# Kernel tuning notes

Measured on AMD Instinct MI355X. Metric: run time of the kernel, lower is better.

## Reference

```python
import jax, jax.numpy as jnp
import numpy as np

D = 1024      # input_dim
NH = 16       # num_heads
HD = D // NH  # head_dim = 64
B, S = 2, 2048


def setup_inputs() -> dict:
    key = jax.random.key(0)
    ks = jax.random.split(key, 12)
    scale = 1.0 / np.sqrt(D)
    inp = {
        "query": jax.random.normal(ks[0], (B, S, D), jnp.float32),
        "key": jax.random.normal(ks[1], (B, S, D), jnp.float32),
        "value": jax.random.normal(ks[2], (B, S, D), jnp.float32),
        # Linear weights stored as [in, out] so y = x @ W + b
        "Wq": jax.random.normal(ks[3], (D, D), jnp.float32) * scale,
        "bq": jnp.zeros((D,), jnp.float32),
        "Wk": jax.random.normal(ks[4], (D, D), jnp.float32) * scale,
        "bk": jnp.zeros((D,), jnp.float32),
        "Wv": jax.random.normal(ks[5], (D, D), jnp.float32) * scale,
        "bv": jnp.zeros((D,), jnp.float32),
        "Wo": jax.random.normal(ks[6], (D, D), jnp.float32) * scale,
        "bo": jnp.zeros((D,), jnp.float32),
    }
    return inp


def reference(query, key, value, Wq, bq, Wk, bk, Wv, bv, Wo, bo):
    b, s, _ = query.shape
    q = query @ Wq + bq
    k = key @ Wk + bk
    v = value @ Wv + bv
    # NOTE: module reshapes to (b, s, head_dim, num_heads) -- heads LAST
    q = q.reshape(b, s, HD, NH)
    k = k.reshape(b, s, HD, NH)
    v = v.reshape(b, s, HD, NH)
    # contract over head_dim d; result [b, l, n, h]
    scores = jnp.einsum('bldh,bndh->blnh', q, k) / jnp.sqrt(jnp.float32(HD))
    # Softmax(dim=-1) in the original acts over the HEAD axis (faithful)
    probs = jax.nn.softmax(scores, axis=-1)
    out = jnp.einsum('blnh,bndh->bldh', probs, v).reshape(b, s, D)
    out = out @ Wo + bo
    return (out, probs)
```

## Files before the change

### kernel.cpp

```cpp
#include <hip/hip_runtime.h>

#define DD   1024
#define NHH  16
#define HDD  64
#define BB   2
#define SS   2048
#define MT   (BB*SS)
#define BL   16
#define BN   32
#define NSPLIT 2

typedef __attribute__((ext_vector_type(8))) __bf16 bf16x8;
typedef __attribute__((ext_vector_type(4))) float  floatx4;
typedef __attribute__((ext_vector_type(4))) short  shortx4;

static __device__ __forceinline__ short bf16_of(float f) {
    unsigned u = __builtin_bit_cast(unsigned, f);
    u = (u + 0x7fffu + ((u >> 16) & 1u)) >> 16;
    return (short)u;
}

static __device__ __forceinline__ void async_copy16(const short* g, short* l) {
    __builtin_amdgcn_global_load_lds(
        (const __attribute__((address_space(1))) unsigned int*)g,
        (__attribute__((address_space(3))) unsigned int*)l,
        16, 0, 0);
}

__global__ void cast_f32_to_bf16(const float* __restrict__ in,
                                 short* __restrict__ out, int n4) {
    int i = blockIdx.x * blockDim.x + threadIdx.x;
    if (i >= n4) return;
    floatx4 f = ((const floatx4*)in)[i];
    shortx4 o;
    o[0] = bf16_of(f[0]); o[1] = bf16_of(f[1]);
    o[2] = bf16_of(f[2]); o[3] = bf16_of(f[3]);
    ((shortx4*)out)[i] = o;
}

__global__ void transpose_cast_w(const float* __restrict__ W,
                                 short* __restrict__ Wt) {
    __shared__ float tile[32][33];
    int tx = threadIdx.x & 31, ty = threadIdx.x >> 5;
    int o0 = blockIdx.x * 32, i0 = blockIdx.y * 32;
#pragma unroll
    for (int r = 0; r < 32; r += 8)
        tile[ty + r][tx] = W[(size_t)(i0 + ty + r) * DD + o0 + tx];
    __syncthreads();
#pragma unroll
    for (int r = 0; r < 32; r += 8)
        Wt[(size_t)(o0 + ty + r) * DD + i0 + tx] = bf16_of(tile[tx][ty + r]);
}

__global__ __launch_bounds__(256) void gemm_tiled(
    const short* __restrict__ X, const short* __restrict__ Wt,
    const float* __restrict__ bias, void* __restrict__ out, int mode) {
    __shared__ short As[128 * 32];
    __shared__ short Bs[64 * 32];
    int t = threadIdx.x;
    int wave = t >> 6, lane = t & 63;
    int quad = lane >> 4, lr = lane & 15;
    int wm = wave & 1, wn = wave >> 1;
    int m0 = blockIdx.x * 128, n0 = blockIdx.y * 64;

    int arow = t >> 2, acol = (t & 3) * 8;
    floatx4 acc[4][2] = {};

    for (int k0 = 0; k0 < DD; k0 += 32) {
        async_copy16(X + (size_t)(m0 + arow) * DD + k0 + acol,       As + t * 8);
        async_copy16(X + (size_t)(m0 + 64 + arow) * DD + k0 + acol,  As + 2048 + t * 8);
        async_copy16(Wt + (size_t)(n0 + arow) * DD + k0 + acol,      Bs + t * 8);
        __syncthreads();
        bf16x8 a[4], bb[2];
#pragma unroll
        for (int mi = 0; mi < 4; mi++)
            a[mi] = *(const bf16x8*)(As + (wm * 64 + mi * 16 + lr) * 32 + quad * 8);
#pragma unroll
        for (int ni = 0; ni < 2; ni++)
            bb[ni] = *(const bf16x8*)(Bs + (wn * 32 + ni * 16 + lr) * 32 + quad * 8);
#pragma unroll
        for (int mi = 0; mi < 4; mi++)
#pragma unroll
            for (int ni = 0; ni < 2; ni++)
                acc[mi][ni] = __builtin_amdgcn_mfma_f32_16x16x32_bf16(
                    a[mi], bb[ni], acc[mi][ni], 0, 0, 0);
        __syncthreads();
    }

#pragma unroll
    for (int mi = 0; mi < 4; mi++)
#pragma unroll
    for (int ni = 0; ni < 2; ni++)
#pragma unroll
    for (int r = 0; r < 4; r++) {
        int m = m0 + wm * 64 + mi * 16 + quad * 4 + r;
        int n = n0 + wn * 32 + ni * 16 + lr;
        float y = acc[mi][ni][r] + bias[n];
        if (mode == 2) {
            ((float*)out)[(size_t)m * DD + n] = y;
        } else {
            int b = m >> 11, l = m & (SS - 1);
            int h = n & (NHH - 1), d = n >> 4;
            size_t idx;
            if (mode == 0) idx = (((size_t)(b * NHH + h) * SS) + l) * HDD + d;
            else           idx = (((size_t)(b * NHH + h) * HDD) + d) * SS + l;
            ((short*)out)[idx] = bf16_of(y);
        }
    }
}

__global__ __launch_bounds__(1024) void attn_fused(
    const short* __restrict__ qws, const short* __restrict__ kws,
    const short* __restrict__ vtws, float* __restrict__ probs,
    float* __restrict__ partial) {
    __shared__ float sm[NHH * 528];
    int h = threadIdx.x >> 6, lane = threadIdx.x & 63;
    int quad = lane >> 4, lr = lane & 15;
    int c    = blockIdx.x & (NSPLIT - 1);
    int l0   = ((blockIdx.x >> 1) & 127) * BL;
    int b    = blockIdx.x >> 8;

    const short* qh = qws  + ((size_t)(b * NHH + h) * SS) * HDD;
    const short* kh = kws  + ((size_t)(b * NHH + h) * SS) * HDD;
    const short* vh = vtws + ((size_t)(b * NHH + h) * HDD) * SS;

    bf16x8 aq0 = *(const bf16x8*)(qh + (size_t)(l0 + lr) * HDD + quad * 8);
    bf16x8 aq1 = *(const bf16x8*)(qh + (size_t)(l0 + lr) * HDD + 32 + quad * 8);

    floatx4 acco[4] = {};
    const int NT = (SS / BN) / NSPLIT;

    for (int nt = c * NT; nt < (c + 1) * NT; nt++) {
        int n0 = nt * BN;
#pragma unroll
        for (int nb = 0; nb < 2; nb++) {
            bf16x8 bk0 = *(const bf16x8*)(kh + (size_t)(n0 + nb * 16 + lr) * HDD + quad * 8);
            bf16x8 bk1 = *(const bf16x8*)(kh + (size_t)(n0 + nb * 16 + lr) * HDD + 32 + quad * 8);
            floatx4 s = {};
            s = __builtin_amdgcn_mfma_f32_16x16x32_bf16(aq0, bk0, s, 0, 0, 0);
            s = __builtin_amdgcn_mfma_f32_16x16x32_bf16(aq1, bk1, s, 0, 0, 0);
#pragma unroll
            for (int r = 0; r < 4; r++) {
                int ll = quad * 4 + r, nn = nb * 16 + lr;
                sm[h * 528 + ll * 33 + nn] = s[r] * 0.125f;
            }
        }
        __syncthreads();
        if (threadIdx.x < BL * BN) {
            int ll = threadIdx.x >> 5, nn = threadIdx.x & 31;
            int base = ll * 33 + nn;
            float p[16];
            float mx = -1e30f;
#pragma unroll
            for (int i = 0; i < 16; i++) { p[i] = sm[i * 528 + base]; mx = fmaxf(mx, p[i]); }
            float sum = 0.f;
#pragma unroll
            for (int i = 0; i < 16; i++) { p[i] = __expf(p[i] - mx); sum += p[i]; }
            float inv = 1.f / sum;
            float* gp = probs + ((size_t)(b * SS + l0 + ll) * SS + n0 + nn) * NHH;
#pragma unroll
            for (int i = 0; i < 16; i++) { p[i] *= inv; sm[i * 528 + base] = p[i]; }
#pragma unroll
            for (int i = 0; i < 4; i++) {
                floatx4 tv; tv[0]=p[4*i]; tv[1]=p[4*i+1]; tv[2]=p[4*i+2]; tv[3]=p[4*i+3];
                ((floatx4*)gp)[i] = tv;
            }
        }
        __syncthreads();
        union { short s[8]; bf16x8 v; } apu;
#pragma unroll
        for (int j = 0; j < 8; j++)
            apu.s[j] = bf16_of(sm[h * 528 + lr * 33 + quad * 8 + j]);
#pragma unroll
        for (int db = 0; db < 4; db++) {
            bf16x8 bv = *(const bf16x8*)(vh + (size_t)(db * 16 + lr) * SS + n0 + quad * 8);
            acco[db] = __builtin_amdgcn_mfma_f32_16x16x32_bf16(apu.v, bv, acco[db], 0, 0, 0);
        }
        __syncthreads();
    }

    float* pc = partial + (size_t)c * MT * DD;
#pragma unroll
    for (int half = 0; half < 2; half++) {
#pragma unroll
        for (int db2 = 0; db2 < 2; db2++) {
            int db = half * 2 + db2;
#pragma unroll
            for (int r = 0; r < 4; r++) {
                int ll = quad * 4 + r;
                int dloc = db2 * 16 + lr;
                sm[ll * 528 + dloc * 16 + h] = acco[db][r];
            }
        }
        __syncthreads();
        int l  = threadIdx.x >> 6;
        int c0 = (threadIdx.x & 63) * 8;
        float* dst = pc + (size_t)(b * SS + l0 + l) * DD + half * 512 + c0;
        const float* srcp = &sm[l * 528 + c0];
        ((floatx4*)dst)[0] = ((const floatx4*)srcp)[0];
        ((floatx4*)dst)[1] = ((const floatx4*)srcp)[1];
        __syncthreads();
    }
}

__global__ void reduce_partials(const float* __restrict__ pa,
                                short* __restrict__ aout) {
    size_t i = (size_t)blockIdx.x * blockDim.x + threadIdx.x;
    floatx4 a = ((const floatx4*)pa)[i];
    floatx4 b = ((const floatx4*)pa)[i + (size_t)MT * DD / 4];
    shortx4 o;
    o[0] = bf16_of(a[0] + b[0]); o[1] = bf16_of(a[1] + b[1]);
    o[2] = bf16_of(a[2] + b[2]); o[3] = bf16_of(a[3] + b[3]);
    ((shortx4*)aout)[i] = o;
}

extern "C" void kernel_launch(void* const* d_in, const int* in_sizes, int n_in,
                              void* d_out, int out_size, void* d_ws, size_t ws_size,
                              hipStream_t stream) {
    const float* query = (const float*)d_in[0];
    const float* key_  = (const float*)d_in[1];
    const float* value = (const float*)d_in[2];
    const float* Wq = (const float*)d_in[3];
    const float* bq = (const float*)d_in[4];
    const float* Wk = (const float*)d_in[5];
    const float* bk = (const float*)d_in[6];
    const float* Wv = (const float*)d_in[7];
    const float* bv = (const float*)d_in[8];
    const float* Wo = (const float*)d_in[9];
    const float* bo = (const float*)d_in[10];

    float* out   = (float*)d_out;
    float* probs = out + (size_t)MT * DD;

    const size_t SZ_X = (size_t)MT * DD;
    const size_t SZ_W = (size_t)DD * DD;
    short* ws   = (short*)d_ws;
    short* wto  = ws;
    short* qws  = wto + SZ_W;
    short* kws  = qws + SZ_X;
    short* vtws = kws + SZ_X;
    short* aout = vtws + SZ_X;
    short* xq   = aout + SZ_X;
    short* xk   = xq + SZ_X;
    short* xv   = xk + SZ_X;
    short* wtq  = xv + SZ_X;
    short* wtk  = wtq + SZ_W;
    short* wtv  = wtk + SZ_W;
    float* partial = (float*)xq;

    int n4 = (int)(SZ_X / 4);
    cast_f32_to_bf16<<<n4 / 256, 256, 0, stream>>>(query, xq, n4);
    cast_f32_to_bf16<<<n4 / 256, 256, 0, stream>>>(key_,  xk, n4);
    cast_f32_to_bf16<<<n4 / 256, 256, 0, stream>>>(value, xv, n4);

    transpose_cast_w<<<dim3(32, 32), 256, 0, stream>>>(Wq, wtq);
    transpose_cast_w<<<dim3(32, 32), 256, 0, stream>>>(Wk, wtk);
    transpose_cast_w<<<dim3(32, 32), 256, 0, stream>>>(Wv, wtv);
    transpose_cast_w<<<dim3(32, 32), 256, 0, stream>>>(Wo, wto);

    gemm_tiled<<<dim3(32, 16), 256, 0, stream>>>(xq, wtq, bq, qws, 0);
    gemm_tiled<<<dim3(32, 16), 256, 0, stream>>>(xk, wtk, bk, kws, 0);
    gemm_tiled<<<dim3(32, 16), 256, 0, stream>>>(xv, wtv, bv, vtws, 1);

    attn_fused<<<BB * (SS / BL) * NSPLIT, 1024, 0, stream>>>(qws, kws, vtws, probs, partial);

    reduce_partials<<<(int)(SZ_X / 4 / 256), 256, 0, stream>>>(partial, aout);

    gemm_tiled<<<dim3(32, 16), 256, 0, stream>>>(aout, wto, bo, out, 2);
}
```

Baseline: 1.061 ms.

## Split attention into score-softmax and PV kernels; permute weights for coalesced head layout

The fused attention kernel is split in two. A score+softmax kernel keeps all 16 heads' scores in registers and writes probs directly, with no LDS round trip or block-wide barriers. A separate PV kernel then re-reads probs from global memory, converts them to bf16 in LDS and multiplies by V. The Q/K/V and O weight rows and columns are permuted during the transpose, so projection outputs land head-contiguous and can be staged through LDS and written as coalesced 16-byte stores. The cost is an extra full read of the large probs tensor, in exchange for better occupancy and fewer synchronisations.

After: 1.133 ms. 6.8% more time.

```diff
diff --git a/kernel.cpp b/kernel.cpp
--- a/kernel.cpp
+++ b/kernel.cpp
@@ -6,13 +6,12 @@
 #define BB   2
 #define SS   2048
 #define MT   (BB*SS)
-#define BL   16
-#define BN   32
 #define NSPLIT 2
 
 typedef __attribute__((ext_vector_type(8))) __bf16 bf16x8;
 typedef __attribute__((ext_vector_type(4))) float  floatx4;
 typedef __attribute__((ext_vector_type(4))) short  shortx4;
+typedef __attribute__((ext_vector_type(4))) int    intx4;
 
 static __device__ __forceinline__ short bf16_of(float f) {
     unsigned u = __builtin_bit_cast(unsigned, f);
@@ -39,17 +38,23 @@
 }
 
 __global__ void transpose_cast_w(const float* __restrict__ W,
-                                 short* __restrict__ Wt) {
+                                 short* __restrict__ Wt, int mode) {
     __shared__ float tile[32][33];
     int tx = threadIdx.x & 31, ty = threadIdx.x >> 5;
     int o0 = blockIdx.x * 32, i0 = blockIdx.y * 32;
 #pragma unroll
-    for (int r = 0; r < 32; r += 8)
-        tile[ty + r][tx] = W[(size_t)(i0 + ty + r) * DD + o0 + tx];
+    for (int r = 0; r < 32; r += 8) {
+        int irow = i0 + ty + r;
+        int srow = (mode == 1) ? (((irow & 63) << 4) | (irow >> 6)) : irow;
+        tile[ty + r][tx] = W[(size_t)srow * DD + o0 + tx];
+    }
     __syncthreads();
 #pragma unroll
-    for (int r = 0; r < 32; r += 8)
-        Wt[(size_t)(o0 + ty + r) * DD + i0 + tx] = bf16_of(tile[tx][ty + r]);
+    for (int r = 0; r < 32; r += 8) {
+        int orow = o0 + ty + r;
+        int drow = (mode == 0) ? (((orow & 15) << 6) | (orow >> 4)) : orow;
+        Wt[(size_t)drow * DD + i0 + tx] = bf16_of(tile[tx][ty + r]);
+    }
 }
 
 __global__ __launch_bounds__(256) void gemm_tiled(
@@ -57,6 +62,7 @@
     const float* __restrict__ bias, void* __restrict__ out, int mode) {
     __shared__ short As[128 * 32];
     __shared__ short Bs[64 * 32];
+    __shared__ __align__(16) short Cs[128 * 72];
     int t = threadIdx.x;
     int wave = t >> 6, lane = t & 63;
     int quad = lane >> 4, lr = lane & 15;
@@ -87,119 +93,165 @@
         __syncthreads();
     }
 
+    if (mode == 2) {
+#pragma unroll
+        for (int mi = 0; mi < 4; mi++)
+#pragma unroll
+        for (int ni = 0; ni < 2; ni++)
+#pragma unroll
+        for (int r = 0; r < 4; r++) {
+            int m = m0 + wm * 64 + mi * 16 + quad * 4 + r;
+            int n = n0 + wn * 32 + ni * 16 + lr;
+            ((float*)out)[(size_t)m * DD + n] = acc[mi][ni][r] + bias[n];
+        }
+        return;
+    }
+
 #pragma unroll
     for (int mi = 0; mi < 4; mi++)
 #pragma unroll
     for (int ni = 0; ni < 2; ni++)
 #pragma unroll
     for (int r = 0; r < 4; r++) {
-        int m = m0 + wm * 64 + mi * 16 + quad * 4 + r;
-        int n = n0 + wn * 32 + ni * 16 + lr;
-        float y = acc[mi][ni][r] + bias[n];
-        if (mode == 2) {
-            ((float*)out)[(size_t)m * DD + n] = y;
-        } else {
-            int b = m >> 11, l = m & (SS - 1);
-            int h = n & (NHH - 1), d = n >> 4;
-            size_t idx;
-            if (mode == 0) idx = (((size_t)(b * NHH + h) * SS) + l) * HDD + d;
-            else           idx = (((size_t)(b * NHH + h) * HDD) + d) * SS + l;
-            ((short*)out)[idx] = bf16_of(y);
+        int nc = wn * 32 + ni * 16 + lr;
+        int np = n0 + nc;
+        float y = acc[mi][ni][r] + bias[((np & 63) << 4) | (np >> 6)];
+        int mr = wm * 64 + mi * 16 + quad * 4 + r;
+        if (mode == 0) Cs[mr * 72 + nc] = bf16_of(y);
+        else           Cs[nc * 136 + mr] = bf16_of(y);
+    }
+    __syncthreads();
+    int b = m0 >> 11, lbase = m0 & (SS - 1);
+    int h = n0 >> 6;
+    short* op = (short*)out;
+    if (mode == 0) {
+        int row = t >> 1, cg = (t & 1) * 32;
+        const intx4* src = (const intx4*)(Cs + row * 72 + cg);
+        intx4* dst = (intx4*)(op + (((size_t)(b * NHH + h) * SS) + lbase + row) * HDD + cg);
+#pragma unroll
+        for (int j = 0; j < 4; j++) dst[j] = src[j];
+    } else {
+        int d = t >> 2, cg = (t & 3) * 32;
+        const intx4* src = (const intx4*)(Cs + d * 136 + cg);
+        intx4* dst = (intx4*)(op + (((size_t)(b * NHH + h) * HDD) + d) * SS + lbase + cg);
+#pragma unroll
+        for (int j = 0; j < 4; j++) dst[j] = src[j];
+    }
+}
+
+__global__ __launch_bounds__(256, 4) void score_softmax(
+    const short* __restrict__ qws, const short* __restrict__ kws,
+    float* __restrict__ probs) {
+    int t = threadIdx.x, wave = t >> 6, lane = t & 63;
+    int quad = lane >> 4, lr = lane & 15;
+    int bid = blockIdx.x;
+    int ntg = bid & 31;
+    int lt  = (bid >> 5) & 127;
+    int b   = bid >> 12;
+    int nt  = ntg * 4 + wave;
+    int l0 = lt * 16, n0 = nt * 16;
+
+    const size_t hstride = (size_t)SS * HDD;
+    const short* qb = qws + (size_t)b * NHH * hstride + (size_t)(l0 + lr) * HDD + quad * 8;
+    const short* kb = kws + (size_t)b * NHH * hstride + (size_t)(n0 + lr) * HDD + quad * 8;
+
+    floatx4 sc[16];
+#pragma unroll
+    for (int h = 0; h < 16; h++) {
+        bf16x8 a0 = *(const bf16x8*)(qb + h * hstride);
+        bf16x8 a1 = *(const bf16x8*)(qb + h * hstride + 32);
+        bf16x8 b0 = *(const bf16x8*)(kb + h * hstride);
+        bf16x8 b1 = *(const bf16x8*)(kb + h * hstride + 32);
+        floatx4 s = {};
+        s = __builtin_amdgcn_mfma_f32_16x16x32_bf16(a0, b0, s, 0, 0, 0);
+        s = __builtin_amdgcn_mfma_f32_16x16x32_bf16(a1, b1, s, 0, 0, 0);
+        s[0] *= 0.125f; s[1] *= 0.125f; s[2] *= 0.125f; s[3] *= 0.125f;
+        sc[h] = s;
+    }
+
+#pragma unroll
+    for (int r = 0; r < 4; r++) {
+        float mx = sc[0][r];
+#pragma unroll
+        for (int h = 1; h < 16; h++) mx = fmaxf(mx, sc[h][r]);
+        float sum = 0.f;
+#pragma unroll
+        for (int h = 0; h < 16; h++) {
+            float e = __expf(sc[h][r] - mx);
+            sc[h][r] = e; sum += e;
         }
-    }
-}
-
-__global__ __launch_bounds__(1024) void attn_fused(
-    const short* __restrict__ qws, const short* __restrict__ kws,
-    const short* __restrict__ vtws, float* __restrict__ probs,
+        float inv = 1.f / sum;
+#pragma unroll
+        for (int h = 0; h < 16; h++) sc[h][r] *= inv;
+    }
+
+#pragma unroll
+    for (int r = 0; r < 4; r++) {
+        float* gp = probs + ((size_t)(b * SS + l0 + quad * 4 + r) * SS + n0 + lr) * NHH;
+#pragma unroll
+        for (int j = 0; j < 4; j++) {
+            floatx4 w;
+            w[0] = sc[4*j+0][r]; w[1] = sc[4*j+1][r];
+            w[2] = sc[4*j+2][r]; w[3] = sc[4*j+3][r];
+            ((floatx4*)gp)[j] = w;
+        }
+    }
+}
+
+__global__ __launch_bounds__(512) void pv_kernel(
+    const float* __restrict__ probs, const short* __restrict__ vtws,
     float* __restrict__ partial) {
-    __shared__ float sm[NHH * 528];
-    int h = threadIdx.x >> 6, lane = threadIdx.x & 63;
+    __shared__ __align__(16) short Ps[16 * 16 * 40];
+    int t = threadIdx.x, wave = t >> 6, lane = t & 63;
     int quad = lane >> 4, lr = lane & 15;
-    int c    = blockIdx.x & (NSPLIT - 1);
-    int l0   = ((blockIdx.x >> 1) & 127) * BL;
-    int b    = blockIdx.x >> 8;
-
-    const short* qh = qws  + ((size_t)(b * NHH + h) * SS) * HDD;
-    const short* kh = kws  + ((size_t)(b * NHH + h) * SS) * HDD;
-    const short* vh = vtws + ((size_t)(b * NHH + h) * HDD) * SS;
-
-    bf16x8 aq0 = *(const bf16x8*)(qh + (size_t)(l0 + lr) * HDD + quad * 8);
-    bf16x8 aq1 = *(const bf16x8*)(qh + (size_t)(l0 + lr) * HDD + 32 + quad * 8);
-
-    floatx4 acco[4] = {};
-    const int NT = (SS / BN) / NSPLIT;
-
-    for (int nt = c * NT; nt < (c + 1) * NT; nt++) {
-        int n0 = nt * BN;
-#pragma unroll
-        for (int nb = 0; nb < 2; nb++) {
-            bf16x8 bk0 = *(const bf16x8*)(kh + (size_t)(n0 + nb * 16 + lr) * HDD + quad * 8);
-            bf16x8 bk1 = *(const bf16x8*)(kh + (size_t)(n0 + nb * 16 + lr) * HDD + 32 + quad * 8);
-            floatx4 s = {};
-            s = __builtin_amdgcn_mfma_f32_16x16x32_bf16(aq0, bk0, s, 0, 0, 0);
-            s = __builtin_amdgcn_mfma_f32_16x16x32_bf16(aq1, bk1, s, 0, 0, 0);
-#pragma unroll
-            for (int r = 0; r < 4; r++) {
-                int ll = quad * 4 + r, nn = nb * 16 + lr;
-                sm[h * 528 + ll * 33 + nn] = s[r] * 0.125f;
+    int cc = blockIdx.x & (NSPLIT - 1);
+    int lt = (blockIdx.x >> 1) & 127;
+    int b  = blockIdx.x >> 8;
+    int l0 = lt * 16;
+    int ls = t >> 5, ns = t & 31;
+
+    const float* gpb = probs + ((size_t)(b * SS + l0 + ls) * SS + ns) * NHH;
+    floatx4 acc[2][4] = {};
+    const int NT = SS / 32 / NSPLIT;
+
+    for (int it = 0; it < NT; it++) {
+        int n0 = (cc * NT + it) * 32;
+        const floatx4* gv = (const floatx4*)(gpb + (size_t)n0 * NHH);
+        floatx4 f0 = gv[0], f1 = gv[1], f2 = gv[2], f3 = gv[3];
+        __syncthreads();
+        short* pw = Ps + ls * 40 + ns;
+        pw[0*640] = bf16_of(f0[0]); pw[1*640] = bf16_of(f0[1]);
+        pw[2*640] = bf16_of(f0[2]); pw[3*640] = bf16_of(f0[3]);
+        pw[4*640] = bf16_of(f1[0]); pw[5*640] = bf16_of(f1[1]);
+        pw[6*640] = bf16_of(f1[2]); pw[7*640] = bf16_of(f1[3]);
+        pw[8*640] = bf16_of(f2[0]); pw[9*640] = bf16_of(f2[1]);
+        pw[10*640] = bf16_of(f2[2]); pw[11*640] = bf16_of(f2[3]);
+        pw[12*640] = bf16_of(f3[0]); pw[13*640] = bf16_of(f3[1]);
+        pw[14*640] = bf16_of(f3[2]); pw[15*640] = bf16_of(f3[3]);
+        __syncthreads();
+#pragma unroll
+        for (int hh = 0; hh < 2; hh++) {
+            int h = wave * 2 + hh;
+            bf16x8 pa = *(const bf16x8*)(Ps + (h * 16 + lr) * 40 + quad * 8);
+            const short* vh = vtws + ((size_t)(b * NHH + h) * HDD) * SS;
+#pragma unroll
+            for (int db = 0; db < 4; db++) {
+                bf16x8 bv = *(const bf16x8*)(vh + (size_t)(db * 16 + lr) * SS + n0 + quad * 8);
+                acc[hh][db] = __builtin_amdgcn_mfma_f32_16x16x32_bf16(pa, bv, acc[hh][db], 0, 0, 0);
             }
         }
-        __syncthreads();
-        if (threadIdx.x < BL * BN) {
-            int ll = threadIdx.x >> 5, nn = threadIdx.x & 31;
-            int base = ll * 33 + nn;
-            float p[16];
-            float mx = -1e30f;
-#pragma unroll
-            for (int i = 0; i < 16; i++) { p[i] = sm[i * 528 + base]; mx = fmaxf(mx, p[i]); }
-            float sum = 0.f;
-#pragma unroll
-            for (int i = 0; i < 16; i++) { p[i] = __expf(p[i] - mx); sum += p[i]; }
-            float inv = 1.f / sum;
-            float* gp = probs + ((size_t)(b * SS + l0 + ll) * SS + n0 + nn) * NHH;
-#pragma unroll
-            for (int i = 0; i < 16; i++) { p[i] *= inv; sm[i * 528 + base] = p[i]; }
-#pragma unroll
-            for (int i = 0; i < 4; i++) {
-                floatx4 tv; tv[0]=p[4*i]; tv[1]=p[4*i+1]; tv[2]=p[4*i+2]; tv[3]=p[4*i+3];
-                ((floatx4*)gp)[i] = tv;
-            }
-        }
-        __syncthreads();
-        union { short s[8]; bf16x8 v; } apu;
-#pragma unroll
-        for (int j = 0; j < 8; j++)
-            apu.s[j] = bf16_of(sm[h * 528 + lr * 33 + quad * 8 + j]);
-#pragma unroll
-        for (int db = 0; db < 4; db++) {
-            bf16x8 bv = *(const bf16x8*)(vh + (size_t)(db * 16 + lr) * SS + n0 + quad * 8);
-            acco[db] = __builtin_amdgcn_mfma_f32_16x16x32_bf16(apu.v, bv, acco[db], 0, 0, 0);
-        }
-        __syncthreads();
-    }
-
-    float* pc = partial + (size_t)c * MT * DD;
-#pragma unroll
-    for (int half = 0; half < 2; half++) {
-#pragma unroll
-        for (int db2 = 0; db2 < 2; db2++) {
-            int db = half * 2 + db2;
-#pragma unroll
-            for (int r = 0; r < 4; r++) {
-                int ll = quad * 4 + r;
-                int dloc = db2 * 16 + lr;
-                sm[ll * 528 + dloc * 16 + h] = acco[db][r];
-            }
-        }
-        __syncthreads();
-        int l  = threadIdx.x >> 6;
-        int c0 = (threadIdx.x & 63) * 8;
-        float* dst = pc + (size_t)(b * SS + l0 + l) * DD + half * 512 + c0;
-        const float* srcp = &sm[l * 528 + c0];
-        ((floatx4*)dst)[0] = ((const floatx4*)srcp)[0];
-        ((floatx4*)dst)[1] = ((const floatx4*)srcp)[1];
-        __syncthreads();
+    }
+
+    float* pc = partial + (size_t)cc * MT * DD;
+#pragma unroll
+    for (int hh = 0; hh < 2; hh++)
+#pragma unroll
+    for (int db = 0; db < 4; db++)
+#pragma unroll
+    for (int r = 0; r < 4; r++) {
+        int h = wave * 2 + hh;
+        pc[((size_t)(b * SS + l0 + quad * 4 + r)) * DD + h * 64 + db * 16 + lr] =
+            acc[hh][db][r];
     }
 }
 
@@ -253,16 +305,18 @@
     cast_f32_to_bf16<<<n4 / 256, 256, 0, stream>>>(key_,  xk, n4);
     cast_f32_to_bf16<<<n4 / 256, 256, 0, stream>>>(value, xv, n4);
 
-    transpose_cast_w<<<dim3(32, 32), 256, 0, stream>>>(Wq, wtq);
-    transpose_cast_w<<<dim3(32, 32), 256, 0, stream>>>(Wk, wtk);
-    transpose_cast_w<<<dim3(32, 32), 256, 0, stream>>>(Wv, wtv);
-    transpose_cast_w<<<dim3(32, 32), 256, 0, stream>>>(Wo, wto);
+    transpose_cast_w<<<dim3(32, 32), 256, 0, stream>>>(Wq, wtq, 0);
+    transpose_cast_w<<<dim3(32, 32), 256, 0, stream>>>(Wk, wtk, 0);
+    transpose_cast_w<<<dim3(32, 32), 256, 0, stream>>>(Wv, wtv, 0);
+    transpose_cast_w<<<dim3(32, 32), 256, 0, stream>>>(Wo, wto, 1);
 
     gemm_tiled<<<dim3(32, 16), 256, 0, stream>>>(xq, wtq, bq, qws, 0);
     gemm_tiled<<<dim3(32, 16), 256, 0, stream>>>(xk, wtk, bk, kws, 0);
     gemm_tiled<<<dim3(32, 16), 256, 0, stream>>>(xv, wtv, bv, vtws, 1);
 
-    attn_fused<<<BB * (SS / BL) * NSPLIT, 1024, 0, stream>>>(qws, kws, vtws, probs, partial);
+    score_softmax<<<BB * 128 * 32, 256, 0, stream>>>(qws, kws, probs);
+
+    pv_kernel<<<BB * 128 * NSPLIT, 512, 0, stream>>>(probs, vtws, partial);
 
     reduce_partials<<<(int)(SZ_X / 4 / 256), 256, 0, stream>>>(partial, aout);
 
```
